# Optimization experiments

Measured on AMD Instinct MI355X. Metric: run time of the kernel, lower is better.

Reference implementation:

```python
import jax, jax.numpy as jnp
import numpy as np

DX, DY, MR, MBAR, NT, B, GOUT = 16, 8, 64, 256, 9, 4, 64
HX, EX, HRNN, HB = 1024, 512, 512, 2048
BB_IN = 1 + EX + HRNN


def setup_inputs() -> dict:
    key = jax.random.key(0)
    ks = jax.random.split(key, 12)
    total = (NT - 1) * MBAR + 1  # 2049 hidden-process time points
    X = jax.random.randint(ks[0], (B, total, DX), 0, 50).astype(jnp.float32)  # molecule counts
    Y = jax.random.normal(ks[1], (B, NT, DY), dtype=jnp.float32)
    # R: cumulative integrated reaction rates (non-decreasing in time)
    R = jnp.cumsum(jax.random.uniform(ks[2], (B, total, MR), dtype=jnp.float32) * 0.01, axis=1)
    stoich = (jax.random.randint(ks[3], (DX, MR), 0, 3) - 1).astype(jnp.float32)  # entries in {-1,0,1}
    times_t = jnp.linspace(0.0, 8.0, NT).astype(jnp.float32)
    times_tau = jnp.linspace(0.0, 1.0, MBAR).astype(jnp.float32)
    sc = lambda k, sh: jax.random.normal(k, sh, dtype=jnp.float32) * np.float32(1.0 / np.sqrt(sh[0]))
    Wx1, bx1 = sc(ks[4], (DX, HX)), jnp.zeros(HX, jnp.float32)
    Wx2, bx2 = sc(ks[5], (HX, EX)), jnp.zeros(EX, jnp.float32)
    Wih = sc(ks[6], (DY, HRNN))
    Whh = sc(ks[7], (HRNN, HRNN))
    bh = jnp.zeros(HRNN, jnp.float32)
    Wb1, bb1 = sc(ks[8], (BB_IN, HB)), jnp.zeros(HB, jnp.float32)
    Wb2, bb2 = sc(ks[9], (HB, GOUT)), jnp.zeros(GOUT, jnp.float32)
    return dict(X=X, Y=Y, R=R, stoich=stoich, times_t=times_t, times_tau=times_tau,
                Wx1=Wx1, bx1=bx1, Wx2=Wx2, bx2=bx2, Wih=Wih, Whh=Whh, bh=bh,
                Wb1=Wb1, bb1=bb1, Wb2=Wb2, bb2=bb2, k=1, k_prime=1, q=0, q_prime=1)


def reference(X, Y, R, stoich, times_t, times_tau,
              Wx1, bx1, Wx2, bx2, Wih, Whh, bh, Wb1, bb1, Wb2, bb2,
              k, k_prime, q, q_prime):
    """stochastic_integral_vectorized: gather displaced states, run the
    martingale network forward on base and displaced states, masked
    accumulation weighted by rate increments. Returns [GOUT]."""
    m_bar = times_tau.shape[0]
    base = k_prime * m_bar

    # --- Y encoder (Elman RNN over the observation slice, final hidden state) ---
    Yslice = Y[q, k + 1:, :]                       # [T_rem, DY]
    def rnn_step(h, y):
        return jnp.tanh(y @ Wih + h @ Whh + bh), None
    eY, _ = jax.lax.scan(rnn_step, jnp.zeros(Whh.shape[0], X.dtype), Yslice)  # [HRNN]

    # --- batched martingale forward: t [N], Xb [N, DX] -> [N, GOUT] ---
    def batched_forward(t, Xb):
        eX = jnp.tanh(Xb @ Wx1 + bx1) @ Wx2 + bx2          # [N, EX]
        eYb = jnp.broadcast_to(eY, (Xb.shape[0], eY.shape[0]))
        inp = jnp.concatenate([t[:, None], eX, eYb], axis=1)  # [N, 1+EX+HRNN]
        return jnp.tanh(inp @ Wb1 + bb1) @ Wb2 + bb2       # [N, GOUT]

    Xbase = X[q_prime, base:base + m_bar, :]               # [M_bar, DX]
    t = times_t[k] + times_tau                              # [M_bar]
    nn = batched_forward(t, Xbase)                          # [M_bar, GOUT]

    mr = stoich.shape[1]
    X_disp = Xbase[None, :, :] + stoich.T[:, None, :]       # [MR, M_bar, DX]
    valid = jnp.all(X_disp >= 0, axis=-1)                   # [MR, M_bar]
    nn_disp = batched_forward(jnp.tile(t, mr),
                              X_disp.reshape(mr * m_bar, -1)).reshape(mr, m_bar, -1)

    R_delta = R[q_prime, base + 1:base + m_bar + 1, :] - R[q_prime, base:base + m_bar, :]  # [M_bar, MR]
    si = jnp.einsum('jmg,mj,jm->g', nn_disp - nn[None], R_delta, valid.astype(nn.dtype))
    return si
```

## Files before the change

kernel.cpp:

```cpp
#include <hip/hip_runtime.h>
#include <math.h>

#define DXc   16
#define MRc   64
#define MBARc 256
#define NTc   9
#define DYc   8
#define HXc   1024
#define EXc   512
#define HRc   512
#define HBc   2048
#define GOUTc 64
#define TOTc  2049

using bf16x8 = __attribute__((ext_vector_type(8))) short;
using f32x4  = __attribute__((ext_vector_type(4))) float;

typedef unsigned int u32;
typedef u32 __attribute__((address_space(1))) gbl_u32;
typedef u32 __attribute__((address_space(3))) lds_u32;

__device__ __forceinline__ float fast_tanh(float x){
    float e = __expf(2.0f * x);
    return 1.0f - 2.0f / (e + 1.0f);
}

__device__ __forceinline__ short f2bf(float f){
    unsigned u = __builtin_bit_cast(unsigned, f);
    u = (u + 0x7FFFu + ((u >> 16) & 1u)) >> 16;
    return (short)u;
}

__device__ __forceinline__ void gld_lds16(const short* g, short* l){
    __builtin_amdgcn_global_load_lds((const gbl_u32*)g, (lds_u32*)l, 16, 0, 0);
}

__global__ void prep_kernel(const float* __restrict__ stoich, const float* __restrict__ Wx1,
                            const float* __restrict__ Wx2, const float* __restrict__ Wb1,
                            const float* __restrict__ X, const float* __restrict__ R,
                            const float* __restrict__ bx1,
                            const int* kpptr, const int* qpptr,
                            float* __restrict__ SW, short* __restrict__ Wx2p,
                            short* __restrict__ Wb1p, float* __restrict__ XW,
                            float* __restrict__ T1, float* __restrict__ wrow,
                            float* __restrict__ hb0){
    int b = blockIdx.x, tid = threadIdx.x;
    if (b < 256){
        int idx = b * 256 + tid;
        int j = idx >> 10, c = idx & 1023;
        float acc = 0.f;
        #pragma unroll
        for (int d = 0; d < DXc; ++d) acc += stoich[d * MRc + j] * Wx1[d * HXc + c];
        SW[idx] = acc;
    } else if (b < 512){
        size_t grp = (size_t)(b - 256) * 256 + tid;
        int lane = grp & 63;
        size_t t2 = grp >> 6;
        int kt = t2 & 31, nt = t2 >> 5;
        int n  = nt * 16 + (lane & 15);
        int k0 = kt * 32 + ((lane >> 4) << 3);
        short o8[8];
        #pragma unroll
        for (int jj = 0; jj < 8; ++jj) o8[jj] = f2bf(Wx2[(size_t)(k0 + jj) * EXc + n]);
        *(bf16x8*)(Wx2p + grp * 8) = *(bf16x8*)o8;
    } else if (b < 1024){
        size_t grp = (size_t)(b - 512) * 256 + tid;
        int lane = grp & 63;
        size_t t2 = grp >> 6;
        int kt = t2 & 15, nt = t2 >> 4;
        int n  = nt * 16 + (lane & 15);
        int k0 = kt * 32 + ((lane >> 4) << 3);
        short o8[8];
        #pragma unroll
        for (int jj = 0; jj < 8; ++jj) o8[jj] = f2bf(Wb1[(size_t)(1 + k0 + jj) * HBc + n]);
        *(bf16x8*)(Wb1p + grp * 8) = *(bf16x8*)o8;
    } else if (b < 2048){
        int idx = (b - 1024) * 256 + tid;
        int m = idx >> 10, c = idx & 1023;
        int base = kpptr[0] * MBARc;
        const float* xr = X + ((size_t)qpptr[0] * TOTc + base + m) * DXc;
        float acc = bx1[c];
        #pragma unroll
        for (int d = 0; d < DXc; ++d) acc += xr[d] * Wx1[d * HXc + c];
        XW[idx] = acc;
        T1[idx] = fast_tanh(acc);
    } else if (b < 2112){
        int j = b - 2048, m = tid;
        int base = kpptr[0] * MBARc;
        int qp = qpptr[0];
        const float* xr = X + ((size_t)qp * TOTc + base + m) * DXc;
        bool valid = true;
        #pragma unroll
        for (int d = 0; d < DXc; ++d) valid = valid && (xr[d] + stoich[d * MRc + j] >= 0.f);
        size_t rb = (size_t)qp * TOTc * MRc;
        float rd = R[rb + (size_t)(base + 1 + m) * MRc + j] - R[rb + (size_t)(base + m) * MRc + j];
        wrow[j * MBARc + m] = valid ? rd : 0.f;
    } else {
        hb0[tid] = 0.f; hb0[tid + 256] = 0.f;
    }
}

__global__ __launch_bounds__(512) void rnn_step_kernel(
    const float* __restrict__ Y, const float* __restrict__ Wih,
    const float* __restrict__ Whh, const float* __restrict__ bh,
    const int* kptr, const int* qptr,
    const float* __restrict__ h_cur, float* __restrict__ h_next, int step){
    __shared__ float hs[HRc];
    __shared__ float psum[8][64];
    int tid = threadIdx.x;
    int o   = tid & 63;
    int seg = tid >> 6;
    int out = blockIdx.x * 64 + o;
    int k = kptr[0], q = qptr[0];
    int t = k + 1 + step;
    hs[tid] = h_cur[tid];
    __syncthreads();
    if (t >= NTc){
        if (seg == 0) h_next[out] = hs[out];
        return;
    }
    int k0 = seg * 64;
    float a0 = 0.f, a1 = 0.f, a2 = 0.f, a3 = 0.f;
    #pragma unroll 4
    for (int kk = 0; kk < 64; kk += 4){
        a0 += hs[k0 + kk + 0] * Whh[(size_t)(k0 + kk + 0) * HRc + out];
        a1 += hs[k0 + kk + 1] * Whh[(size_t)(k0 + kk + 1) * HRc + out];
        a2 += hs[k0 + kk + 2] * Whh[(size_t)(k0 + kk + 2) * HRc + out];
        a3 += hs[k0 + kk + 3] * Whh[(size_t)(k0 + kk + 3) * HRc + out];
    }
    psum[seg][o] = (a0 + a1) + (a2 + a3);
    __syncthreads();
    if (seg == 0){
        float a = 0.f;
        #pragma unroll
        for (int r = 0; r < 8; ++r) a += psum[r][o];
        const float* y = Y + (q * NTc + t) * DYc;
        float z = bh[out];
        #pragma unroll
        for (int d = 0; d < DYc; ++d) z += y[d] * Wih[d * HRc + out];
        h_next[out] = fast_tanh(z + a);
    }
}

__global__ __launch_bounds__(256) void cyex_kernel(const float* __restrict__ eY,
                                                   const float* __restrict__ Wb1,
                                                   const float* __restrict__ bb1,
                                                   const float* __restrict__ T1,
                                                   const float* __restrict__ Wx2,
                                                   const float* __restrict__ bx2,
                                                   float* __restrict__ cY,
                                                   float* __restrict__ eXb){
    __shared__ float t1s[8 * 1024];
    int b = blockIdx.x, tid = threadIdx.x;
    if (b < 8){
        int h = b * 256 + tid;
        float acc = bb1[h];
        for (int e = 0; e < EXc; ++e) acc += eY[e] * Wb1[(size_t)(1 + EXc + e) * HBc + h];
        cY[h] = acc;
        return;
    }
    int b2 = b - 8;
    int e = (b2 & 1) * 256 + tid;
    int m0 = (b2 >> 1) * 8;
    #pragma unroll
    for (int l = 0; l < 32; ++l){
        int idx = tid + l * 256;
        t1s[idx] = T1[(size_t)(m0 + (idx >> 10)) * HXc + (idx & 1023)];
    }
    __syncthreads();
    float acc[8] = {};
    for (int kk = 0; kk < HXc; ++kk){
        float wv = Wx2[(size_t)kk * EXc + e];
        #pragma unroll
        for (int mm = 0; mm < 8; ++mm) acc[mm] += t1s[mm * 1024 + kk] * wv;
    }
    float be = bx2[e];
    #pragma unroll
    for (int mm = 0; mm < 8; ++mm) eXb[(size_t)(m0 + mm) * EXc + e] = acc[mm] + be;
}

__global__ __launch_bounds__(256) void z2base_kernel(const float* __restrict__ eXb,
                                                     const float* __restrict__ Wb1,
                                                     const float* __restrict__ cY,
                                                     const float* __restrict__ times_t,
                                                     const float* __restrict__ times_tau,
                                                     const int* kptr,
                                                     float* __restrict__ TB){
    __shared__ float exs[8 * 512];
    int tid = threadIdx.x;
    int h = blockIdx.x * 256 + tid;
    int m0 = blockIdx.y * 8;
    #pragma unroll
    for (int l = 0; l < 16; ++l){
        int idx = tid + l * 256;
        exs[idx] = eXb[(size_t)(m0 + (idx >> 9)) * EXc + (idx & 511)];
    }
    __syncthreads();
    float acc[8] = {};
    for (int kk = 0; kk < EXc; ++kk){
        float wv = Wb1[(size_t)(1 + kk) * HBc + h];
        #pragma unroll
        for (int mm = 0; mm < 8; ++mm) acc[mm] += exs[mm * 512 + kk] * wv;
    }
    float tk = times_t[kptr[0]];
    float w0 = Wb1[h], cy = cY[h];
    #pragma unroll
    for (int mm = 0; mm < 8; ++mm){
        int m = m0 + mm;
        float z = acc[mm] + (tk + times_tau[m]) * w0 + cy;
        TB[(size_t)m * HBc + h] = fast_tanh(z);
    }
}

__global__ void act_delta_kernel(const float* __restrict__ XW, const float* __restrict__ T1,
                                 const float* __restrict__ SW, short* __restrict__ A1p){
    size_t grp = (size_t)blockIdx.x * 256 + threadIdx.x;
    int lane = grp & 63;
    size_t t2 = grp >> 6;
    int kt = t2 & 31;
    int mt = (int)(t2 >> 5);
    int m  = mt * 16 + (lane & 15);
    int c0 = kt * 32 + ((lane >> 4) << 3);
    int j    = m >> 8;
    int mloc = m & 255;
    const float* xwr = XW + (size_t)mloc * HXc + c0;
    const float* t1r = T1 + (size_t)mloc * HXc + c0;
    const float* swr = SW + (size_t)j * HXc + c0;
    short o8[8];
    #pragma unroll
    for (int i = 0; i < 8; ++i)
        o8[i] = f2bf(fast_tanh(xwr[i] + swr[i]) - t1r[i]);
    *(bf16x8*)(A1p + grp * 8) = *(bf16x8*)o8;
}

#define MMGRID(aa, bb) {                                                       \
    _Pragma("unroll") for (int i_ = 0; i_ < 4; ++i_)                           \
        _Pragma("unroll") for (int j_ = 0; j_ < 4; ++j_)                       \
            acc[i_][j_] = __builtin_amdgcn_mfma_f32_16x16x32_bf16(aa[i_], bb[j_], acc[i_][j_], 0, 0, 0); }

__device__ __forceinline__ void stage64(const short* __restrict__ Ap, const short* __restrict__ Bp,
                                        short* As, short* Bs,
                                        int at0, int bt0, int s, int KTOT, int wave, int lane){
    #pragma unroll
    for (int c = 0; c < 8; ++c){
        int ci = wave * 8 + c;
        int half = ci >> 4;
        int t    = (ci >> 1) & 7;
        int kt   = ci & 1;
        const short* src = half ? (Bp + ((size_t)(bt0 + t) * KTOT + (2 * s + kt)) * 512 + lane * 8)
                                : (Ap + ((size_t)(at0 + t) * KTOT + (2 * s + kt)) * 512 + lane * 8);
        short* dst = (half ? Bs : As) + (t * 2 + kt) * 512;
        gld_lds16(src, dst);
    }
}

#define STAGE_COMPUTE(As, Bs) {                                                       \
    _Pragma("unroll") for (int kt_ = 0; kt_ < 2; ++kt_){                              \
        bf16x8 af[4], bfr[4];                                                         \
        _Pragma("unroll") for (int i_ = 0; i_ < 4; ++i_)                              \
            af[i_] = *(const bf16x8*)((As) + (((wm * 4 + i_) * 2 + kt_) * 512) + lane * 8); \
        _Pragma("unroll") for (int j_ = 0; j_ < 4; ++j_)                              \
            bfr[j_] = *(const bf16x8*)((Bs) + (((wn * 4 + j_) * 2 + kt_) * 512) + lane * 8); \
        MMGRID(af, bfr);                                                              \
    } }

__global__ __launch_bounds__(256) void gemm1_s(
    const short* __restrict__ Ap, const short* __restrict__ Bp,
    short* __restrict__ dXp){
    const int KTOT = 32, S = 16;
    __shared__ __align__(16) short Asb[2][8192];
    __shared__ __align__(16) short Bsb[2][8192];
    int tid = threadIdx.x;
    int wave = tid >> 6, lane = tid & 63;
    int wm = wave >> 1, wn = wave & 1;
    int bn = blockIdx.x, bm = blockIdx.y;
    int quad = lane >> 4, llo = lane & 15;
    f32x4 acc[4][4];
    #pragma unroll
    for (int i = 0; i < 4; ++i)
        #pragma unroll
        for (int j = 0; j < 4; ++j) acc[i][j] = (f32x4){0.f, 0.f, 0.f, 0.f};
    stage64(Ap, Bp, Asb[0], Bsb[0], bm * 8, bn * 8, 0, KTOT, wave, lane);
    for (int s = 0; s < S; ++s){
        int buf = s & 1;
        __syncthreads();
        if (s + 1 < S)
            stage64(Ap, Bp, Asb[buf ^ 1], Bsb[buf ^ 1], bm * 8, bn * 8, s + 1, KTOT, wave, lane);
        STAGE_COMPUTE(Asb[buf], Bsb[buf]);
    }
    #pragma unroll
    for (int j = 0; j < 4; ++j){
        int e = bn * 128 + wn * 64 + j * 16 + llo;
        int kt2 = e >> 5, hi2 = (e >> 3) & 3, jj = e & 7;
        #pragma unroll
        for (int i = 0; i < 4; ++i){
            #pragma unroll
            for (int r = 0; r < 4; ++r){
                int m = bm * 128 + wm * 64 + i * 16 + quad * 4 + r;
                int mt2 = m >> 4, lo2 = m & 15;
                dXp[(((size_t)mt2 * 16 + kt2) * 64 + hi2 * 16 + lo2) * 8 + jj] =
                    f2bf(acc[i][j][r]);
            }
        }
    }
}

__global__ __launch_bounds__(256) void gemm2_s(
    const short* __restrict__ Ap, const short* __restrict__ Bp,
    const float* __restrict__ TB, const float* __restrict__ wrow,
    float* __restrict__ dacc){
    const int KTOT = 16, S = 8;
    __shared__ __align__(16) short Asb[2][8192];
    __shared__ __align__(16) short Bsb[2][8192];
    int tid = threadIdx.x;
    int wave = tid >> 6, lane = tid & 63;
    int wm = wave >> 1, wn = wave & 1;
    int bn = blockIdx.x, bm = blockIdx.y;
    int quad = lane >> 4, llo = lane & 15;
    f32x4 acc[4][4];
    #pragma unroll
    for (int i = 0; i < 4; ++i)
        #pragma unroll
        for (int j = 0; j < 4; ++j) acc[i][j] = (f32x4){0.f, 0.f, 0.f, 0.f};
    stage64(Ap, Bp, Asb[0], Bsb[0], bm * 8, bn * 8, 0, KTOT, wave, lane);
    for (int s = 0; s < S; ++s){
        int buf = s & 1;
        __syncthreads();
        if (s + 1 < S)
            stage64(Ap, Bp, Asb[buf ^ 1], Bsb[buf ^ 1], bm * 8, bn * 8, s + 1, KTOT, wave, lane);
        STAGE_COMPUTE(Asb[buf], Bsb[buf]);
    }
    int nj[4];
    #pragma unroll
    for (int j = 0; j < 4; ++j) nj[j] = bn * 128 + wn * 64 + j * 16 + llo;
    float part[4] = {0.f, 0.f, 0.f, 0.f};
    #pragma unroll
    for (int i = 0; i < 4; ++i){
        #pragma unroll
        for (int r = 0; r < 4; ++r){
            int m = bm * 128 + wm * 64 + i * 16 + quad * 4 + r;
            float wr = wrow[m];
            const float* trow = TB + (size_t)(m & 255) * HBc;
            #pragma unroll
            for (int j = 0; j < 4; ++j){
                float tb  = trow[nj[j]];
                float tdz = fast_tanh(acc[i][j][r]);
                float num = tdz * (1.0f - tb * tb);
                float den = 1.0f + tb * tdz;
                part[j] += wr * num * __builtin_amdgcn_rcpf(den);
            }
        }
    }
    #pragma unroll
    for (int j = 0; j < 4; ++j){
        part[j] += __shfl_xor(part[j], 16);
        part[j] += __shfl_xor(part[j], 32);
    }
    __shared__ float redn[128];
    if (tid < 128) redn[tid] = 0.f;
    __syncthreads();
    if (lane < 16){
        #pragma unroll
        for (int j = 0; j < 4; ++j)
            atomicAdd(&redn[wn * 64 + j * 16 + llo], part[j]);
    }
    __syncthreads();
    if (tid < 128) atomicAdd(&dacc[bn * 128 + tid], redn[tid]);
}

__global__ void out_kernel(const float* __restrict__ dacc, const float* __restrict__ Wb2,
                           float* __restrict__ out){
    __shared__ float red[4][64];
    int tid = threadIdx.x;
    int g = tid & 63, seg = tid >> 6;
    int h0 = blockIdx.x * 256 + seg * 64;
    float s = 0.f;
    #pragma unroll 8
    for (int hh = 0; hh < 64; ++hh)
        s += dacc[h0 + hh] * Wb2[(size_t)(h0 + hh) * GOUTc + g];
    red[seg][g] = s;
    __syncthreads();
    if (tid < 64)
        atomicAdd(&out[tid], red[0][tid] + red[1][tid] + red[2][tid] + red[3][tid]);
}

extern "C" void kernel_launch(void* const* d_in, const int* in_sizes, int n_in,
                              void* d_out, int out_size, void* d_ws, size_t ws_size,
                              hipStream_t stream){
    const float* X         = (const float*)d_in[0];
    const float* Y         = (const float*)d_in[1];
    const float* R         = (const float*)d_in[2];
    const float* stoich    = (const float*)d_in[3];
    const float* times_t   = (const float*)d_in[4];
    const float* times_tau = (const float*)d_in[5];
    const float* Wx1 = (const float*)d_in[6];
    const float* bx1 = (const float*)d_in[7];
    const float* Wx2 = (const float*)d_in[8];
    const float* bx2 = (const float*)d_in[9];
    const float* Wih = (const float*)d_in[10];
    const float* Whh = (const float*)d_in[11];
    const float* bh  = (const float*)d_in[12];
    const float* Wb1 = (const float*)d_in[13];
    const float* bb1 = (const float*)d_in[14];
    const float* Wb2 = (const float*)d_in[15];
    const int* kp  = (const int*)d_in[17];
    const int* kpp = (const int*)d_in[18];
    const int* qp  = (const int*)d_in[19];
    const int* qpp = (const int*)d_in[20];
    float* out = (float*)d_out;

    float* ws   = (float*)d_ws;
    float* hb0  = ws;
    float* hb1  = ws + 512;
    float* cY   = ws + 1024;
    float* dacc = ws + 3072;
    float* wrow = ws + 5120;
    float* SW   = ws + 21504;
    float* XW   = ws + 87040;
    float* T1   = ws + 349184;
    float* eXb  = ws + 611328;
    float* TB   = ws + 742400;
    short* A1p  = (short*)(ws + 1266688);
    short* Wx2p = (short*)(ws + 9655296);
    short* Wb1p = (short*)(ws + 9917440);
    short* dXp  = (short*)(ws + 10441728);

    hipMemsetAsync(dacc, 0, HBc * sizeof(float), stream);
    hipMemsetAsync(out,  0, GOUTc * sizeof(float), stream);
    prep_kernel     <<<2113, 256, 0, stream>>>(stoich, Wx1, Wx2, Wb1, X, R, bx1, kpp, qpp,
                                               SW, Wx2p, Wb1p, XW, T1, wrow, hb0);
    act_delta_kernel<<<8192, 256, 0, stream>>>(XW, T1, SW, A1p);
    for (int s = 0; s < 8; ++s){
        const float* hc = (s & 1) ? hb1 : hb0;
        float*       hn = (s & 1) ? hb0 : hb1;
        rnn_step_kernel<<<8, 512, 0, stream>>>(Y, Wih, Whh, bh, kp, qp, hc, hn, s);
    }
    cyex_kernel     <<<72,   256, 0, stream>>>(hb0, Wb1, bb1, T1, Wx2, bx2, cY, eXb);
    z2base_kernel   <<<dim3(8, 32), 256, 0, stream>>>(eXb, Wb1, cY, times_t, times_tau, kp, TB);
    gemm1_s         <<<dim3(4, 128),  256, 0, stream>>>(A1p, Wx2p, dXp);
    gemm2_s         <<<dim3(16, 128), 256, 0, stream>>>(dXp, Wb1p, TB, wrow, dacc);
    out_kernel      <<<8,    256, 0, stream>>>(dacc, Wb2, out);
}
```

Baseline: 355.6 us.

## Split-K the base-path GEMMs with atomics and fold memsets into prep

The base-path eX and z2 matmuls, previously run on few blocks (64 and 256) with long K loops, are now split along K across 512 blocks each and accumulate partial results into pre-initialised buffers with atomicAdd. The cY computation gets its own kernel with a 4-way K split and an LDS reduction, and a separate tb_kernel applies the time term, bias and tanh. The two hipMemsetAsync calls are replaced by zeroing and bias initialisation inside prep_kernel. The aim is more parallelism in latency-bound small kernels, at the cost of atomic traffic, an extra launch, and non-deterministic float summation order.

```diff
diff --git a/kernel.cpp b/kernel.cpp
--- a/kernel.cpp
+++ b/kernel.cpp
@@ -38,12 +38,14 @@
 __global__ void prep_kernel(const float* __restrict__ stoich, const float* __restrict__ Wx1,
                             const float* __restrict__ Wx2, const float* __restrict__ Wb1,
                             const float* __restrict__ X, const float* __restrict__ R,
-                            const float* __restrict__ bx1,
+                            const float* __restrict__ bx1, const float* __restrict__ bx2,
                             const int* kpptr, const int* qpptr,
                             float* __restrict__ SW, short* __restrict__ Wx2p,
                             short* __restrict__ Wb1p, float* __restrict__ XW,
                             float* __restrict__ T1, float* __restrict__ wrow,
-                            float* __restrict__ hb0){
+                            float* __restrict__ hb0, float* __restrict__ dacc,
+                            float* __restrict__ outz, float* __restrict__ eXb,
+                            float* __restrict__ Z2Bacc){
     int b = blockIdx.x, tid = threadIdx.x;
     if (b < 256){
         int idx = b * 256 + tid;
@@ -95,8 +97,16 @@
         size_t rb = (size_t)qp * TOTc * MRc;
         float rd = R[rb + (size_t)(base + 1 + m) * MRc + j] - R[rb + (size_t)(base + m) * MRc + j];
         wrow[j * MBARc + m] = valid ? rd : 0.f;
+    } else if (b == 2112){
+        hb0[tid] = 0.f; hb0[tid + 256] = 0.f;
+        #pragma unroll
+        for (int l = 0; l < 8; ++l) dacc[tid + l * 256] = 0.f;
+        if (tid < GOUTc) outz[tid] = 0.f;
+    } else if (b < 2625){
+        int idx = (b - 2113) * 256 + tid;
+        eXb[idx] = bx2[idx & 511];
     } else {
-        hb0[tid] = 0.f; hb0[tid + 256] = 0.f;
+        Z2Bacc[(size_t)(b - 2625) * 256 + tid] = 0.f;
     }
 }
 
@@ -142,74 +152,85 @@
     }
 }
 
-__global__ __launch_bounds__(256) void cyex_kernel(const float* __restrict__ eY,
-                                                   const float* __restrict__ Wb1,
-                                                   const float* __restrict__ bb1,
-                                                   const float* __restrict__ T1,
-                                                   const float* __restrict__ Wx2,
-                                                   const float* __restrict__ bx2,
-                                                   float* __restrict__ cY,
-                                                   float* __restrict__ eXb){
-    __shared__ float t1s[8 * 1024];
+__global__ __launch_bounds__(256) void cy_kernel(const float* __restrict__ eY,
+                                                 const float* __restrict__ Wb1,
+                                                 const float* __restrict__ bb1,
+                                                 float* __restrict__ cY){
+    __shared__ float psum[4][64];
+    int tid = threadIdx.x;
+    int o = tid & 63, seg = tid >> 6;
+    int h = blockIdx.x * 64 + o;
+    int e0 = seg * 128;
+    float acc = 0.f;
+    #pragma unroll 4
+    for (int e = 0; e < 128; ++e)
+        acc += eY[e0 + e] * Wb1[(size_t)(1 + EXc + e0 + e) * HBc + h];
+    psum[seg][o] = acc;
+    __syncthreads();
+    if (seg == 0)
+        cY[h] = bb1[h] + psum[0][o] + psum[1][o] + psum[2][o] + psum[3][o];
+}
+
+__global__ __launch_bounds__(256) void exbase_kernel(const float* __restrict__ T1,
+                                                     const float* __restrict__ Wx2,
+                                                     float* __restrict__ eXb){
+    __shared__ float t1s[8 * 128];
     int b = blockIdx.x, tid = threadIdx.x;
-    if (b < 8){
-        int h = b * 256 + tid;
-        float acc = bb1[h];
-        for (int e = 0; e < EXc; ++e) acc += eY[e] * Wb1[(size_t)(1 + EXc + e) * HBc + h];
-        cY[h] = acc;
-        return;
-    }
-    int b2 = b - 8;
-    int e = (b2 & 1) * 256 + tid;
-    int m0 = (b2 >> 1) * 8;
-    #pragma unroll
-    for (int l = 0; l < 32; ++l){
+    int mg = b & 31, eh = (b >> 5) & 1, kq = b >> 6;
+    int m0 = mg * 8, e = eh * 256 + tid, k0 = kq * 128;
+    #pragma unroll
+    for (int l = 0; l < 4; ++l){
         int idx = tid + l * 256;
-        t1s[idx] = T1[(size_t)(m0 + (idx >> 10)) * HXc + (idx & 1023)];
+        t1s[idx] = T1[(size_t)(m0 + (idx >> 7)) * HXc + k0 + (idx & 127)];
     }
     __syncthreads();
     float acc[8] = {};
-    for (int kk = 0; kk < HXc; ++kk){
-        float wv = Wx2[(size_t)kk * EXc + e];
-        #pragma unroll
-        for (int mm = 0; mm < 8; ++mm) acc[mm] += t1s[mm * 1024 + kk] * wv;
-    }
-    float be = bx2[e];
-    #pragma unroll
-    for (int mm = 0; mm < 8; ++mm) eXb[(size_t)(m0 + mm) * EXc + e] = acc[mm] + be;
-}
-
-__global__ __launch_bounds__(256) void z2base_kernel(const float* __restrict__ eXb,
-                                                     const float* __restrict__ Wb1,
-                                                     const float* __restrict__ cY,
-                                                     const float* __restrict__ times_t,
-                                                     const float* __restrict__ times_tau,
-                                                     const int* kptr,
-                                                     float* __restrict__ TB){
-    __shared__ float exs[8 * 512];
-    int tid = threadIdx.x;
-    int h = blockIdx.x * 256 + tid;
-    int m0 = blockIdx.y * 8;
-    #pragma unroll
-    for (int l = 0; l < 16; ++l){
+    #pragma unroll 4
+    for (int kk = 0; kk < 128; ++kk){
+        float wv = Wx2[(size_t)(k0 + kk) * EXc + e];
+        #pragma unroll
+        for (int mm = 0; mm < 8; ++mm) acc[mm] += t1s[mm * 128 + kk] * wv;
+    }
+    #pragma unroll
+    for (int mm = 0; mm < 8; ++mm)
+        atomicAdd(&eXb[(size_t)(m0 + mm) * EXc + e], acc[mm]);
+}
+
+__global__ __launch_bounds__(256) void z2acc_kernel(const float* __restrict__ eXb,
+                                                    const float* __restrict__ Wb1,
+                                                    float* __restrict__ Z2Bacc){
+    __shared__ float exs[8 * 256];
+    int b = blockIdx.x, tid = threadIdx.x;
+    int mg = b & 31, hh = (b >> 5) & 7, kq = b >> 8;
+    int m0 = mg * 8, h = hh * 256 + tid, k0 = kq * 256;
+    #pragma unroll
+    for (int l = 0; l < 8; ++l){
         int idx = tid + l * 256;
-        exs[idx] = eXb[(size_t)(m0 + (idx >> 9)) * EXc + (idx & 511)];
+        exs[idx] = eXb[(size_t)(m0 + (idx >> 8)) * EXc + k0 + (idx & 255)];
     }
     __syncthreads();
     float acc[8] = {};
-    for (int kk = 0; kk < EXc; ++kk){
-        float wv = Wb1[(size_t)(1 + kk) * HBc + h];
-        #pragma unroll
-        for (int mm = 0; mm < 8; ++mm) acc[mm] += exs[mm * 512 + kk] * wv;
-    }
+    #pragma unroll 4
+    for (int kk = 0; kk < 256; ++kk){
+        float wv = Wb1[(size_t)(1 + k0 + kk) * HBc + h];
+        #pragma unroll
+        for (int mm = 0; mm < 8; ++mm) acc[mm] += exs[mm * 256 + kk] * wv;
+    }
+    #pragma unroll
+    for (int mm = 0; mm < 8; ++mm)
+        atomicAdd(&Z2Bacc[(size_t)(m0 + mm) * HBc + h], acc[mm]);
+}
+
+__global__ void tb_kernel(const float* __restrict__ Z2Bacc, const float* __restrict__ Wb1,
+                          const float* __restrict__ cY, const float* __restrict__ times_t,
+                          const float* __restrict__ times_tau, const int* kptr,
+                          float* __restrict__ TB){
+    int b = blockIdx.x, tid = threadIdx.x;
+    int m = b >> 3, h = (b & 7) * 256 + tid;
     float tk = times_t[kptr[0]];
-    float w0 = Wb1[h], cy = cY[h];
-    #pragma unroll
-    for (int mm = 0; mm < 8; ++mm){
-        int m = m0 + mm;
-        float z = acc[mm] + (tk + times_tau[m]) * w0 + cy;
-        TB[(size_t)m * HBc + h] = fast_tanh(z);
-    }
+    size_t idx = (size_t)m * HBc + h;
+    float z = Z2Bacc[idx] + (tk + times_tau[m]) * Wb1[h] + cY[h];
+    TB[idx] = fast_tanh(z);
 }
 
 __global__ void act_delta_kernel(const float* __restrict__ XW, const float* __restrict__ T1,
@@ -409,34 +430,36 @@
     const int* qpp = (const int*)d_in[20];
     float* out = (float*)d_out;
 
-    float* ws   = (float*)d_ws;
-    float* hb0  = ws;
-    float* hb1  = ws + 512;
-    float* cY   = ws + 1024;
-    float* dacc = ws + 3072;
-    float* wrow = ws + 5120;
-    float* SW   = ws + 21504;
-    float* XW   = ws + 87040;
-    float* T1   = ws + 349184;
-    float* eXb  = ws + 611328;
-    float* TB   = ws + 742400;
-    short* A1p  = (short*)(ws + 1266688);
-    short* Wx2p = (short*)(ws + 9655296);
-    short* Wb1p = (short*)(ws + 9917440);
-    short* dXp  = (short*)(ws + 10441728);
-
-    hipMemsetAsync(dacc, 0, HBc * sizeof(float), stream);
-    hipMemsetAsync(out,  0, GOUTc * sizeof(float), stream);
-    prep_kernel     <<<2113, 256, 0, stream>>>(stoich, Wx1, Wx2, Wb1, X, R, bx1, kpp, qpp,
-                                               SW, Wx2p, Wb1p, XW, T1, wrow, hb0);
+    float* ws     = (float*)d_ws;
+    float* hb0    = ws;
+    float* hb1    = ws + 512;
+    float* cY     = ws + 1024;
+    float* dacc   = ws + 3072;
+    float* wrow   = ws + 5120;
+    float* SW     = ws + 21504;
+    float* XW     = ws + 87040;
+    float* T1     = ws + 349184;
+    float* eXb    = ws + 611328;
+    float* TB     = ws + 742400;
+    float* Z2Bacc = ws + 1266688;
+    short* A1p    = (short*)(ws + 1790976);
+    short* Wx2p   = (short*)(ws + 10179584);
+    short* Wb1p   = (short*)(ws + 10441728);
+    short* dXp    = (short*)(ws + 10966016);
+
+    prep_kernel     <<<4673, 256, 0, stream>>>(stoich, Wx1, Wx2, Wb1, X, R, bx1, bx2, kpp, qpp,
+                                               SW, Wx2p, Wb1p, XW, T1, wrow, hb0, dacc, out,
+                                               eXb, Z2Bacc);
     act_delta_kernel<<<8192, 256, 0, stream>>>(XW, T1, SW, A1p);
     for (int s = 0; s < 8; ++s){
         const float* hc = (s & 1) ? hb1 : hb0;
         float*       hn = (s & 1) ? hb0 : hb1;
         rnn_step_kernel<<<8, 512, 0, stream>>>(Y, Wih, Whh, bh, kp, qp, hc, hn, s);
     }
-    cyex_kernel     <<<72,   256, 0, stream>>>(hb0, Wb1, bb1, T1, Wx2, bx2, cY, eXb);
-    z2base_kernel   <<<dim3(8, 32), 256, 0, stream>>>(eXb, Wb1, cY, times_t, times_tau, kp, TB);
+    cy_kernel       <<<32,   256, 0, stream>>>(hb0, Wb1, bb1, cY);
+    exbase_kernel   <<<512,  256, 0, stream>>>(T1, Wx2, eXb);
+    z2acc_kernel    <<<512,  256, 0, stream>>>(eXb, Wb1, Z2Bacc);
+    tb_kernel       <<<2048, 256, 0, stream>>>(Z2Bacc, Wb1, cY, times_t, times_tau, kp, TB);
     gemm1_s         <<<dim3(4, 128),  256, 0, stream>>>(A1p, Wx2p, dXp);
     gemm2_s         <<<dim3(16, 128), 256, 0, stream>>>(dXp, Wb1p, TB, wrow, dacc);
     out_kernel      <<<8,    256, 0, stream>>>(dacc, Wb2, out);
```

Measured after the change: 297.2 us. 16.4% less time.
